# Performance work log

Hardware: AMD Instinct MI355X
Metric: run time of the kernel (lower is better)

Reference implementation:

```python
import jax, jax.numpy as jnp
import numpy as np
from jax.scipy.special import gammaln, logsumexp

S, K, O, H = 64, 16, 32, 30   # state_dim, act_dim, obs_dim, horizon
T, N = 200, 512               # seq len, batch
EPS = 1e-6
LOG2PI = float(np.log(2.0 * np.pi))
NUM_PARAMS = S * O * 2 + K * S * S + S + S + 1


def setup_inputs() -> dict:
    key = jax.random.key(0)
    k1, k2, k3 = jax.random.split(key, 3)
    o = jax.random.normal(k1, (T, N, O), dtype=jnp.float32)
    a = jax.random.randint(k2, (T, N), 0, K)
    theta = jax.random.normal(k3, (N, NUM_PARAMS), dtype=jnp.float32)
    return {"o": o, "a": a, "theta": theta}


def _transform_params(theta):
    sizes = [S * O * 2, K * S * S, S, S, 1]
    idx = np.cumsum(sizes)[:-1]
    tA, tB, tC, tD, ttau = jnp.split(theta, idx, axis=-1)
    A_mean, A_lv = jnp.split(tA, 2, axis=-1)
    A_mean = A_mean.reshape(-1, S, O)
    A_std = jax.nn.softplus(A_lv.reshape(-1, S, O)) + EPS  # rectify
    B = jax.nn.softmax(tB.reshape(-1, K, S, S), axis=-1)
    C = jax.nn.softmax(tC.reshape(-1, 1, S), axis=-1)
    D = jax.nn.softmax(tD.reshape(-1, S), axis=-1)
    tau = jax.nn.sigmoid(ttau) * (2.0 * H) + 1.0  # [N,1]
    return A_mean, A_std, B, C, D, tau


def reference(o, a, theta):
    A_mean, A_std, B, C, D, tau = _transform_params(theta)

    # --- negative expected free energy reward: r[n,k,i] ---
    ent = jnp.sum(0.5 + 0.5 * LOG2PI + jnp.log(A_std), axis=-1)          # Normal entropy, [N,S]
    kl = jnp.sum(B * (jnp.log(B + EPS) - jnp.log(C[:, None] + EPS)), -1)  # KL(B || C), [N,K,S]
    eh = jnp.einsum('nkij,nj->nki', B, ent)
    r = -kl - eh

    # --- finite-horizon value iteration: q [H,N,K,S] ---
    def vi_step(qt, _):
        v = logsumexp(qt, axis=-2)                    # [N,S]
        qn = r + jnp.einsum('nkij,nj->nki', B, v)
        return qn, qn
    _, q_rest = jax.lax.scan(vi_step, r, None, length=H - 1)
    q = jnp.concatenate([r[None], q_rest], axis=0)

    # --- truncated poisson horizon weights: pdf [N,H] ---
    hh = jnp.arange(H, dtype=jnp.float32)
    logp_h = hh[None, :] * jnp.log(tau) - tau - gammaln(hh + 1.0)[None, :]
    pdf = jnp.exp(logp_h)
    pdf = pdf / jnp.sum(pdf, axis=-1, keepdims=True)

    batch_idx = jnp.arange(N)

    def time_step(b, inp):
        o_t, a_t = inp
        # policy from current belief
        qb = jnp.einsum('ni,hnki->hnk', b, q)
        pi_h = jax.nn.softmax(qb, axis=-1)
        pi_t = jnp.einsum('hnk,nh->nk', pi_h, pdf)
        # belief update
        B_a = B[batch_idx, a_t]                       # [N,S,S]
        s = jnp.einsum('nij,ni->nj', B_a, b)
        logp_s = jnp.log(s + EPS)
        lp = -0.5 * ((o_t[:, None, :] - A_mean) / A_std) ** 2 \
             - jnp.log(A_std) - 0.5 * LOG2PI          # [N,S,O]
        joint = logp_s + jnp.sum(lp, axis=-1)         # [N,S]
        b_next = jax.nn.softmax(joint, axis=-1)
        logp_o = logsumexp(joint, axis=-1)
        return b_next, (pi_t, b, logp_o)

    _, (pi, b_seq, logp_o) = jax.lax.scan(time_step, D, (o, a))
    return pi, b_seq, logp_o
```

## Files before the change

### kernel.cpp

```cpp
#include <hip/hip_runtime.h>
#include <hip/hip_bf16.h>
#include <math.h>

#define SDIM 64
#define KDIM 16
#define ODIM 32
#define HDIM 30
#define TDIM 200
#define NDIM 512
#define NP 69761
#define EPSV 1e-6f
#define LOG2PIF 1.8378770664093453f

__device__ __forceinline__ float softplusf(float x) {
    return (x > 0.f) ? x + log1pf(expf(-x)) : log1pf(expf(x));
}
__device__ __forceinline__ float wave_max64(float v) {
#pragma unroll
    for (int off = 32; off; off >>= 1) v = fmaxf(v, __shfl_xor(v, off, 64));
    return v;
}
__device__ __forceinline__ float wave_sum64(float v) {
#pragma unroll
    for (int off = 32; off; off >>= 1) v += __shfl_xor(v, off, 64);
    return v;
}
__device__ __forceinline__ void bar_lds() {
    asm volatile("s_waitcnt lgkmcnt(0)\n\ts_barrier" ::: "memory");
}

__global__ __launch_bounds__(256) void transform_kernel(
    const float* __restrict__ theta, float* __restrict__ invstd,
    float* __restrict__ c0, float* __restrict__ ent,
    float* __restrict__ logC, float* __restrict__ Dws,
    float* __restrict__ pdfws)
{
    __shared__ float ls[SDIM * 33];
    const int n = blockIdx.x, tid = threadIdx.x;
    const float* thn = theta + (size_t)n * NP;

    for (int idx = tid; idx < SDIM * ODIM; idx += 256) {
        float x = thn[2048 + idx];
        float sp = softplusf(x) + EPSV;
        invstd[(size_t)n * SDIM * ODIM + idx] = 1.f / sp;
        int s = idx >> 5, oo = idx & 31;
        ls[s * 33 + oo] = logf(sp);
    }
    __syncthreads();

    const int wave = tid >> 6, lane = tid & 63;
    if (wave == 0) {
        float sum = 0.f;
#pragma unroll
        for (int oo = 0; oo < ODIM; ++oo) sum += ls[lane * 33 + oo];
        c0[n * SDIM + lane]  = -sum - 16.f * LOG2PIF;
        ent[n * SDIM + lane] =  sum + 32.f * (0.5f + 0.5f * LOG2PIF);
    } else if (wave == 1) {
        float x = thn[69632 + lane];
        float m = wave_max64(x);
        float e = expf(x - m);
        float ssum = wave_sum64(e);
        logC[n * SDIM + lane] = logf(e / ssum + EPSV);
    } else if (wave == 2) {
        float x = thn[69696 + lane];
        float m = wave_max64(x);
        float e = expf(x - m);
        float ssum = wave_sum64(e);
        Dws[n * SDIM + lane] = e / ssum;
    } else {
        float tt = thn[69760];
        float tau = 60.f / (1.f + expf(-tt)) + 1.f;
        float p = 0.f;
        if (lane < HDIM)
            p = expf((float)lane * logf(tau) - tau - lgammaf((float)lane + 1.f));
        float ssum = wave_sum64(p);
        if (lane < HDIM) pdfws[n * HDIM + lane] = p / ssum;
    }
}

__global__ __launch_bounds__(256) void row_stats_kernel(
    const float* __restrict__ theta, const float* __restrict__ logC,
    const float* __restrict__ ent, float* __restrict__ lse,
    float* __restrict__ rws, __hip_bfloat16* __restrict__ bn)
{
    const int gw = blockIdx.x * 4 + (threadIdx.x >> 6);
    const int lane = threadIdx.x & 63;
    const int n = gw >> 10, rl = gw & 1023;
    float x = theta[(size_t)n * NP + 4096 + (size_t)rl * 64 + lane];
    float m = wave_max64(x);
    float e = expf(x - m);
    float ssum = wave_sum64(e);
    float Bj = e / ssum;
    if (bn) {
        const int k = rl >> 6, i = rl & 63;
        __hip_bfloat16 h = __float2bfloat16(Bj);
        unsigned short bits;
        __builtin_memcpy(&bits, &h, 2);
        ((unsigned short*)bn)[(size_t)n * KDIM * SDIM * SDIM
            + (size_t)k * 4096 + (size_t)(i >> 1) * 128 + lane * 2 + (i & 1)] = bits;
    }
    float contrib = Bj * (logf(Bj + EPSV) - logC[n * SDIM + lane] + ent[n * SDIM + lane]);
    contrib = wave_sum64(contrib);
    if (lane == 0) {
        lse[gw] = m + logf(ssum);
        rws[gw] = -contrib;
    }
}

#define Z2PART(TT_, BUF_) do {                                                 \
    const int ob_ = (wave - 1) * 8;                                            \
    const float* om_ = &o_s[(TT_) * ODIM + ob_];                               \
    float zz_ = 0.f;                                                           \
    _Pragma("unroll")                                                          \
    for (int j_ = 0; j_ < 8; ++j_) {                                           \
        float z_ = (om_[j_] - mean_s[lane * 33 + ob_ + j_])                    \
                 * istd_s[lane * 33 + ob_ + j_];                               \
        zz_ += z_ * z_;                                                        \
    }                                                                          \
    z2p_s[BUF_][wave - 1][lane] = zz_;                                         \
} while (0)

#define BSTEPF(T_, U_) do {                                                    \
    const int cur_ = (T_) & 1, nxt_ = cur_ ^ 1;                                \
    float ecz_ = 0.f, cm_ = 0.f;                                               \
    if (wave >= 1) {                                                           \
        float aA_ = 0.f, aB_ = 0.f;                                            \
        _Pragma("unroll")                                                      \
        for (int ii = 0; ii < 10; ii += 2) {                                   \
            if (ii < nrow)     aA_ += er[ii]     * b_bc[cur_][rbase + ii];     \
            if (ii + 1 < nrow) aB_ += er[ii + 1] * b_bc[cur_][rbase + ii + 1]; \
        }                                                                      \
        part_s[wave - 1][lane] = aA_ + aB_;                                    \
        if (wave == 6) out_b[((size_t)(T_) * NDIM + n) * SDIM + lane] = b_bc[cur_][lane]; \
    } else {                                                                   \
        float z2_ = z2p_s[cur_][0][lane] + z2p_s[cur_][1][lane]                \
                  + z2p_s[cur_][2][lane] + z2p_s[cur_][3][lane];               \
        float c_ = c0_r - 0.5f * z2_;                                          \
        cm_ = wave_max64(c_);                                                  \
        ecz_ = __expf(c_ - cm_);                                               \
    }                                                                          \
    bar_lds();                                             \
    if (wave == 0) {                                                           \
        float sv_ = part_s[0][lane] + part_s[1][lane] + part_s[2][lane]        \
                  + part_s[3][lane] + part_s[4][lane] + part_s[5][lane]        \
                  + part_s[6][lane];                                           \
        float u_ = (sv_ + EPSV) * ecz_;                                        \
        float S_ = wave_sum64(u_);                                             \
        b_bc[nxt_][lane] = u_ / S_;                                            \
        if (lane == 0) out_lp[(size_t)(T_) * NDIM + n] = cm_ + __logf(S_);     \
    } else {                                                                   \
        if ((T_) + 1 < TDIM) {                                                 \
            _Pragma("unroll")                                                  \
            for (int m_ = 0; m_ < 5; ++m_) {                                   \
                if (2 * m_ < nrow)                                             \
                    er[2 * m_] = __uint_as_float(U_[m_] << 16);                \
                if (2 * m_ + 1 < nrow)                                         \
                    er[2 * m_ + 1] = __uint_as_float(U_[m_] & 0xffff0000u);    \
            }                                                                  \
            if (wave <= 4) Z2PART((T_) + 1, nxt_);                             \
        }                                                                      \
        const int tl_ = ((T_) + 3 < TDIM) ? (T_) + 3 : TDIM - 1;               \
        const uint* up_ = bnn32 + (size_t)a_s[tl_] * 2048 + (rbase >> 1) * 64 + lane; \
        _Pragma("unroll")                                                      \
        for (int m_ = 0; m_ < 5; ++m_)                                         \
            if (2 * m_ < nrow) U_[m_] = up_[m_ * 64];                          \
    }                                                                          \
    bar_lds();                                                 \
} while (0)

__global__ __launch_bounds__(512) void belief_fast_kernel(
    const float* __restrict__ o, const int* __restrict__ a,
    const float* __restrict__ theta, const __hip_bfloat16* __restrict__ bn,
    const float* __restrict__ invstd, const float* __restrict__ c0g,
    const float* __restrict__ Dws,
    float* __restrict__ out_b, float* __restrict__ out_lp)
{
    __shared__ float o_s[TDIM * ODIM];
    __shared__ int   a_s[TDIM];
    __shared__ float mean_s[SDIM * 33];
    __shared__ float istd_s[SDIM * 33];
    __shared__ float c0_sh[SDIM];
    __shared__ __align__(16) float b_bc[2][SDIM];
    __shared__ float part_s[7][68];
    __shared__ float z2p_s[2][4][SDIM];

    const int n = blockIdx.x, tid = threadIdx.x;
    const int wave = tid >> 6, lane = tid & 63;
    const float* thn = theta + (size_t)n * NP;
    const uint* bnn32 = (const uint*)(bn + (size_t)n * KDIM * SDIM * SDIM);

    for (int idx = tid; idx < TDIM * ODIM; idx += 512)
        o_s[idx] = o[((size_t)(idx >> 5) * NDIM + n) * ODIM + (idx & 31)];
    if (tid < TDIM) a_s[tid] = a[tid * NDIM + n];
    for (int idx = tid; idx < SDIM * ODIM; idx += 512) {
        int s = idx >> 5, oo = idx & 31;
        mean_s[s * 33 + oo] = thn[idx];
        istd_s[s * 33 + oo] = invstd[(size_t)n * SDIM * ODIM + idx];
    }
    if (tid < SDIM) { c0_sh[tid] = c0g[n * SDIM + tid]; b_bc[0][tid] = Dws[n * SDIM + tid]; }
    __syncthreads();

    const float c0_r = (wave == 0) ? c0_sh[lane] : 0.f;
    const int rbase = (wave >= 1) ? (wave - 1) * 10 : 0;
    const int nrow  = (wave >= 1) ? ((SDIM - rbase) < 10 ? (SDIM - rbase) : 10) : 0;

    float er[10];
    uint u0[5], u1[5];
    if (wave >= 1) {
        const uint* p0 = bnn32 + (size_t)a_s[0] * 2048 + (rbase >> 1) * 64 + lane;
#pragma unroll
        for (int m = 0; m < 5; ++m) if (2 * m < nrow) u0[m] = p0[m * 64];
#pragma unroll
        for (int m = 0; m < 5; ++m) {
            if (2 * m < nrow)     er[2 * m]     = __uint_as_float(u0[m] << 16);
            if (2 * m + 1 < nrow) er[2 * m + 1] = __uint_as_float(u0[m] & 0xffff0000u);
        }
        const uint* p1 = bnn32 + (size_t)a_s[1] * 2048 + (rbase >> 1) * 64 + lane;
#pragma unroll
        for (int m = 0; m < 5; ++m) if (2 * m < nrow) u0[m] = p1[m * 64];
        const uint* p2 = bnn32 + (size_t)a_s[2] * 2048 + (rbase >> 1) * 64 + lane;
#pragma unroll
        for (int m = 0; m < 5; ++m) if (2 * m < nrow) u1[m] = p2[m * 64];
        if (wave <= 4) Z2PART(0, 0);
    }
    __syncthreads();

#pragma unroll 1
    for (int t = 0; t < TDIM; t += 2) {
        BSTEPF(t, u0);
        BSTEPF(t + 1, u1);
    }
}

#define BSTEP(T_, RAW_) do {                                                   \
    const int cur_ = (T_) & 1, nxt_ = cur_ ^ 1;                                \
    if (wave >= 1) {                                                           \
        float acc_ = 0.f;                                                      \
        _Pragma("unroll")                                                      \
        for (int ii = 0; ii < 10; ++ii)                                        \
            if (ii < nrow) acc_ += er[ii] * b_s[cur_][rbase + ii];             \
        part_s[wave - 1][lane] = acc_;                                         \
        if (wave == 6) out_b[((size_t)(T_) * NDIM + n) * SDIM + lane] = b_s[cur_][lane]; \
    }                                                                          \
    bar_lds();                                                                 \
    if (wave == 0) {                                                           \
        float sv_ = part_s[0][lane] + part_s[1][lane] + part_s[2][lane]        \
                  + part_s[3][lane] + part_s[4][lane] + part_s[5][lane]        \
                  + part_s[6][lane];                                           \
        float z2_ = z2p_s[cur_][0][lane] + z2p_s[cur_][1][lane]                \
                  + z2p_s[cur_][2][lane] + z2p_s[cur_][3][lane];               \
        float joint_ = __logf(sv_ + EPSV) + c0_s[lane] - 0.5f * z2_;           \
        float m_ = wave_max64(joint_);                                         \
        float e_ = __expf(joint_ - m_);                                        \
        float ss_ = wave_sum64(e_);                                            \
        b_s[nxt_][lane] = e_ / ss_;                                            \
        if (lane == 0) out_lp[(size_t)(T_) * NDIM + n] = m_ + __logf(ss_);     \
    } else {                                                                   \
        if ((T_) + 1 < TDIM) {                                                 \
            const int an_ = a_s[(T_) + 1];                                     \
            const float* ln_ = lseA + an_ * SDIM;                              \
            _Pragma("unroll")                                                  \
            for (int ii = 0; ii < 10; ++ii)                                    \
                if (ii < nrow) er[ii] = __expf(RAW_[ii] - ln_[rbase + ii]);    \
            if (wave <= 4) Z2PART((T_) + 1, nxt_);                             \
        }                                                                      \
        const int tl_ = ((T_) + 3 < TDIM) ? (T_) + 3 : TDIM - 1;               \
        const int a3_ = a_s[tl_];                                              \
        const float* X3_ = Xn + (size_t)a3_ * SDIM * SDIM;                     \
        _Pragma("unroll")                                                      \
        for (int ii = 0; ii < 10; ++ii)                                        \
            if (ii < nrow) RAW_[ii] = X3_[(size_t)(rbase + ii) * SDIM + lane]; \
    }                                                                          \
    bar_lds();                                                                 \
} while (0)

__global__ __launch_bounds__(512) void belief_kernel(
    const float* __restrict__ o, const int* __restrict__ a,
    const float* __restrict__ theta, const float* __restrict__ lse,
    const float* __restrict__ invstd, const float* __restrict__ c0g,
    const float* __restrict__ Dws,
    float* __restrict__ out_b, float* __restrict__ out_lp)
{
    __shared__ float o_s[TDIM * ODIM];
    __shared__ int   a_s[TDIM];
    __shared__ float mean_s[SDIM * 33];
    __shared__ float istd_s[SDIM * 33];
    __shared__ float lseA[KDIM * SDIM];
    __shared__ float c0_s[SDIM];
    __shared__ float b_s[2][SDIM];
    __shared__ float part_s[7][68];
    __shared__ float z2p_s[2][4][SDIM];

    const int n = blockIdx.x, tid = threadIdx.x;
    const int wave = tid >> 6, lane = tid & 63;
    const float* thn = theta + (size_t)n * NP;
    const float* Xn  = thn + 4096;

    for (int idx = tid; idx < TDIM * ODIM; idx += 512)
        o_s[idx] = o[((size_t)(idx >> 5) * NDIM + n) * ODIM + (idx & 31)];
    if (tid < TDIM) a_s[tid] = a[tid * NDIM + n];
    for (int idx = tid; idx < SDIM * ODIM; idx += 512) {
        int s = idx >> 5, oo = idx & 31;
        mean_s[s * 33 + oo] = thn[idx];
        istd_s[s * 33 + oo] = invstd[(size_t)n * SDIM * ODIM + idx];
    }
    for (int idx = tid; idx < KDIM * SDIM; idx += 512)
        lseA[idx] = lse[(size_t)n * KDIM * SDIM + idx];
    if (tid < SDIM) { c0_s[tid] = c0g[n * SDIM + tid]; b_s[0][tid] = Dws[n * SDIM + tid]; }
    __syncthreads();

    const int rbase = (wave >= 1) ? (wave - 1) * 10 : 0;
    const int nrow  = (wave >= 1) ? ((SDIM - rbase) < 10 ? (SDIM - rbase) : 10) : 0;

    float er[10], raw0[10], raw1[10];
    if (wave >= 1) {
        const int a0 = a_s[0];
        const float* X0 = Xn + (size_t)a0 * SDIM * SDIM;
        const float* l0 = lseA + a0 * SDIM;
#pragma unroll
        for (int ii = 0; ii < 10; ++ii)
            if (ii < nrow) er[ii] = __expf(X0[(size_t)(rbase + ii) * SDIM + lane] - l0[rbase + ii]);
        const int a1 = a_s[1];
        const float* X1 = Xn + (size_t)a1 * SDIM * SDIM;
#pragma unroll
        for (int ii = 0; ii < 10; ++ii)
            if (ii < nrow) raw0[ii] = X1[(size_t)(rbase + ii) * SDIM + lane];
        const int a2 = a_s[2];
        const float* X2 = Xn + (size_t)a2 * SDIM * SDIM;
#pragma unroll
        for (int ii = 0; ii < 10; ++ii)
            if (ii < nrow) raw1[ii] = X2[(size_t)(rbase + ii) * SDIM + lane];
        if (wave <= 4) Z2PART(0, 0);
    }
    __syncthreads();

#pragma unroll 1
    for (int t = 0; t < TDIM; t += 2) {
        BSTEP(t, raw0);
        BSTEP(t + 1, raw1);
    }
}

__global__ __launch_bounds__(512) void vi_kernel(
    const float* __restrict__ theta, const float* __restrict__ lse,
    const float* __restrict__ rws, float* __restrict__ q_ws)
{
    __shared__ float q_lds[KDIM * 68];
    __shared__ __align__(16) float v_lds[68];
    const int n = blockIdx.x, tid = threadIdx.x;
    const float* Xn = theta + (size_t)n * NP + 4096;

    const float l0  = lse[(size_t)n * 1024 + tid];
    const float l1  = lse[(size_t)n * 1024 + 512 + tid];
    const float rr0 = rws[(size_t)n * 1024 + tid];
    const float rr1 = rws[(size_t)n * 1024 + 512 + tid];

    float4 er0[16], er1[16];
    {
        const float* X0 = Xn + (size_t)tid * 64;
        const float* X1 = Xn + (size_t)(512 + tid) * 64;
#pragma unroll
        for (int j = 0; j < 16; ++j) {
            float4 x = *(const float4*)(X0 + j * 4);
            er0[j] = make_float4(__expf(x.x - l0), __expf(x.y - l0),
                                 __expf(x.z - l0), __expf(x.w - l0));
            float4 y = *(const float4*)(X1 + j * 4);
            er1[j] = make_float4(__expf(y.x - l1), __expf(y.y - l1),
                                 __expf(y.z - l1), __expf(y.w - l1));
        }
    }

    float qr0 = rr0, qr1 = rr1;
    float* qw = q_ws + (size_t)n * HDIM * 1024;
    const int kq0 = tid >> 6, iq = tid & 63;
    qw[tid] = qr0;
    qw[512 + tid] = qr1;
    q_lds[kq0 * 68 + iq] = qr0;
    q_lds[(8 + kq0) * 68 + iq] = qr1;
    __syncthreads();

#pragma unroll 1
    for (int h = 1; h < HDIM; ++h) {
        if (tid < 64) {
            float m = -1e30f;
#pragma unroll
            for (int k = 0; k < KDIM; ++k) m = fmaxf(m, q_lds[k * 68 + tid]);
            float s = 0.f;
#pragma unroll
            for (int k = 0; k < KDIM; ++k) s += __expf(q_lds[k * 68 + tid] - m);
            v_lds[tid] = m + __logf(s);
        }
        bar_lds();
        float a0x = 0.f, a0y = 0.f, a0z = 0.f, a0w = 0.f;
        float a1x = 0.f, a1y = 0.f, a1z = 0.f, a1w = 0.f;
#pragma unroll
        for (int jq = 0; jq < 16; ++jq) {
            const float4 v4 = *(const float4*)&v_lds[jq * 4];
            a0x += er0[jq].x * v4.x; a0y += er0[jq].y * v4.y;
            a0z += er0[jq].z * v4.z; a0w += er0[jq].w * v4.w;
            a1x += er1[jq].x * v4.x; a1y += er1[jq].y * v4.y;
            a1z += er1[jq].z * v4.z; a1w += er1[jq].w * v4.w;
        }
        qr0 = rr0 + ((a0x + a0y) + (a0z + a0w));
        qr1 = rr1 + ((a1x + a1y) + (a1z + a1w));
        qw[(size_t)h * 1024 + tid] = qr0;
        qw[(size_t)h * 1024 + 512 + tid] = qr1;
        q_lds[kq0 * 68 + iq] = qr0;
        q_lds[(8 + kq0) * 68 + iq] = qr1;
        bar_lds();
    }
}

__global__ __launch_bounds__(512, 1) void policy_bc_kernel(
    const float* __restrict__ q_ws, const float* __restrict__ out_b_g,
    const float* __restrict__ pdfg, float* __restrict__ out_pi)
{
    __shared__ __align__(16) float b_all[TDIM * SDIM];
    __shared__ float part[2][8][16];
    __shared__ float pdf_s[32];

    const int n = blockIdx.x, tid = threadIdx.x;
    const int w = tid >> 6, lane = tid & 63;
    const int hl = lane >> 4, kk = lane & 15;
    const int hown = w * 4 + hl;
    const float* qn = q_ws + (size_t)n * HDIM * 1024;

    for (int idx = tid; idx < TDIM * 16; idx += 512) {
        const int t = idx >> 4, jq = idx & 15;
        *(float4*)&b_all[t * SDIM + jq * 4] =
            *(const float4*)&out_b_g[((size_t)t * NDIM + n) * SDIM + jq * 4];
    }
    if (tid < 32) pdf_s[tid] = (tid < HDIM) ? pdfg[n * HDIM + tid] : 0.f;

    float4 qrow[16];
    if (hown < HDIM) {
#pragma unroll
        for (int jq = 0; jq < 16; ++jq)
            qrow[jq] = *(const float4*)&qn[(size_t)hown * 1024 + kk * 64 + jq * 4];
    } else {
#pragma unroll
        for (int jq = 0; jq < 16; ++jq)
            qrow[jq] = make_float4(0.f, 0.f, 0.f, 0.f);
    }
    __syncthreads();
    const float pdfh = pdf_s[hown];

#pragma unroll 1
    for (int t = 0; t < TDIM; ++t) {
        const int cur = t & 1;
        const float* br = &b_all[t * SDIM];
        float ax = 0.f, ay = 0.f, az = 0.f, aw = 0.f;
#pragma unroll
        for (int jq = 0; jq < 16; ++jq) {
            const float4 b4 = *(const float4*)&br[jq * 4];
            ax += qrow[jq].x * b4.x; ay += qrow[jq].y * b4.y;
            az += qrow[jq].z * b4.z; aw += qrow[jq].w * b4.w;
        }
        float acc = (ax + ay) + (az + aw);
        float m = acc;
        m = fmaxf(m, __shfl_xor(m, 1, 64));
        m = fmaxf(m, __shfl_xor(m, 2, 64));
        m = fmaxf(m, __shfl_xor(m, 4, 64));
        m = fmaxf(m, __shfl_xor(m, 8, 64));
        float e = __expf(acc - m);
        float S = e;
        S += __shfl_xor(S, 1, 64);
        S += __shfl_xor(S, 2, 64);
        S += __shfl_xor(S, 4, 64);
        S += __shfl_xor(S, 8, 64);
        float val = pdfh * e / S;
        val += __shfl_xor(val, 16, 64);
        val += __shfl_xor(val, 32, 64);
        if (lane < 16) part[cur][w][lane] = val;
        if (w == 0 && t > 0 && lane < 16) {
            const int prv = cur ^ 1;
            float s8 = 0.f;
#pragma unroll
            for (int ww = 0; ww < 8; ++ww) s8 += part[prv][ww][lane];
            out_pi[((size_t)(t - 1) * NDIM + n) * KDIM + lane] = s8;
        }
        bar_lds();
    }
    if (w == 0 && lane < 16) {
        float s8 = 0.f;
#pragma unroll
        for (int ww = 0; ww < 8; ++ww) s8 += part[(TDIM - 1) & 1][ww][lane];
        out_pi[((size_t)(TDIM - 1) * NDIM + n) * KDIM + lane] = s8;
    }
}

__global__ __launch_bounds__(512) void vi_policy_kernel(
    const float* __restrict__ theta, const float* __restrict__ lse,
    const float* __restrict__ rws, const float* __restrict__ pdfg,
    const float* __restrict__ out_b_g, float* __restrict__ out_pi)
{
    __shared__ __align__(16) float q_s[HDIM * KDIM * 68];
    __shared__ float r_s[KDIM * SDIM];
    __shared__ float lse_s[KDIM * SDIM];
    __shared__ __align__(16) float v_s[SDIM];
    __shared__ __align__(16) float b_lds[64 * 68];
    __shared__ float pdf_s[32];

    const int n = blockIdx.x, tid = threadIdx.x;
    const int wave = tid >> 6, lane = tid & 63;
    const int sub = lane & 15, rq = lane >> 4;
    const float* Xn = theta + (size_t)n * NP + 4096;

    for (int idx = tid; idx < KDIM * SDIM; idx += 512) {
        r_s[idx]   = rws[(size_t)n * KDIM * SDIM + idx];
        lse_s[idx] = lse[(size_t)n * KDIM * SDIM + idx];
    }
    if (tid < HDIM) pdf_s[tid] = pdfg[n * HDIM + tid];
    __syncthreads();

    for (int idx = tid; idx < KDIM * SDIM; idx += 512)
        q_s[(idx >> 6) * 68 + (idx & 63)] = r_s[idx];

    float4 breg[32];
#pragma unroll
    for (int it = 0; it < 32; ++it) {
        const int row = it * 32 + wave * 4 + rq;
        const float* xr = Xn + (size_t)row * SDIM + sub * 4;
        const float l = lse_s[row];
        breg[it] = make_float4(__expf(xr[0] - l), __expf(xr[1] - l),
                               __expf(xr[2] - l), __expf(xr[3] - l));
    }
    bar_lds();

#pragma unroll 1
    for (int h = 1; h < HDIM; ++h) {
        if (tid < SDIM) {
            const int base = (h - 1) * KDIM;
            float m = -1e30f;
#pragma unroll
            for (int k = 0; k < KDIM; ++k) m = fmaxf(m, q_s[(base + k) * 68 + tid]);
            float ssum = 0.f;
#pragma unroll
            for (int k = 0; k < KDIM; ++k) ssum += __expf(q_s[(base + k) * 68 + tid] - m);
            v_s[tid] = m + __logf(ssum);
        }
        bar_lds();
        const float4 v4 = *(const float4*)&v_s[sub * 4];
#pragma unroll
        for (int it = 0; it < 32; ++it) {
            const int row = it * 32 + wave * 4 + rq;
            float acc = breg[it].x * v4.x + breg[it].y * v4.y
                      + breg[it].z * v4.z + breg[it].w * v4.w;
            acc += __shfl_xor(acc, 1, 64);
            acc += __shfl_xor(acc, 2, 64);
            acc += __shfl_xor(acc, 4, 64);
            acc += __shfl_xor(acc, 8, 64);
            if (sub == 0)
                q_s[(h * KDIM + (row >> 6)) * 68 + (row & 63)] = r_s[row] + acc;
        }
        bar_lds();
    }

    const int tc = tid >> 4, kk = tid & 15;
#pragma unroll 1
    for (int t0 = 0; t0 < TDIM; t0 += 64) {
        const int nt = (TDIM - t0) < 64 ? (TDIM - t0) : 64;
        for (int idx = tid; idx < nt * 16; idx += 512) {
            const int row = idx >> 4, jq = idx & 15;
            *(float4*)&b_lds[row * 68 + jq * 4] =
                *(const float4*)&out_b_g[(((size_t)(t0 + row)) * NDIM + n) * SDIM + jq * 4];
        }
        bar_lds();
        const bool vA = tc < nt, vB = (tc + 32) < nt;
        float4 bqA[16], bqB[16];
        if (vA) {
#pragma unroll
            for (int jq = 0; jq < 16; ++jq)
                bqA[jq] = *(const float4*)&b_lds[tc * 68 + jq * 4];
        }
        if (vB) {
#pragma unroll
            for (int jq = 0; jq < 16; ++jq)
                bqB[jq] = *(const float4*)&b_lds[(tc + 32) * 68 + jq * 4];
        }
        float pikA = 0.f, pikB = 0.f;
#pragma unroll 1
        for (int h = 0; h < HDIM; ++h) {
            const float* qr = &q_s[(h * KDIM + kk) * 68];
            float aA = 0.f, aB = 0.f;
#pragma unroll
            for (int jq = 0; jq < 16; ++jq) {
                const float4 qv = *(const float4*)&qr[jq * 4];
                if (vA) aA += qv.x * bqA[jq].x + qv.y * bqA[jq].y
                            + qv.z * bqA[jq].z + qv.w * bqA[jq].w;
                if (vB) aB += qv.x * bqB[jq].x + qv.y * bqB[jq].y
                            + qv.z * bqB[jq].z + qv.w * bqB[jq].w;
            }
            float mA = aA, mB = aB;
            mA = fmaxf(mA, __shfl_xor(mA, 1, 64));
            mA = fmaxf(mA, __shfl_xor(mA, 2, 64));
            mA = fmaxf(mA, __shfl_xor(mA, 4, 64));
            mA = fmaxf(mA, __shfl_xor(mA, 8, 64));
            mB = fmaxf(mB, __shfl_xor(mB, 1, 64));
            mB = fmaxf(mB, __shfl_xor(mB, 2, 64));
            mB = fmaxf(mB, __shfl_xor(mB, 4, 64));
            mB = fmaxf(mB, __shfl_xor(mB, 8, 64));
            float eA = __expf(aA - mA), eB = __expf(aB - mB);
            float SA = eA, SB = eB;
            SA += __shfl_xor(SA, 1, 64);
            SA += __shfl_xor(SA, 2, 64);
            SA += __shfl_xor(SA, 4, 64);
            SA += __shfl_xor(SA, 8, 64);
            SB += __shfl_xor(SB, 1, 64);
            SB += __shfl_xor(SB, 2, 64);
            SB += __shfl_xor(SB, 4, 64);
            SB += __shfl_xor(SB, 8, 64);
            const float ph = pdf_s[h];
            pikA += ph * eA / SA;
            pikB += ph * eB / SB;
        }
        if (vA) out_pi[(((size_t)(t0 + tc)) * NDIM + n) * KDIM + kk] = pikA;
        if (vB) out_pi[(((size_t)(t0 + 32 + tc)) * NDIM + n) * KDIM + kk] = pikB;
        bar_lds();
    }
}

extern "C" void kernel_launch(void* const* d_in, const int* in_sizes, int n_in,
                              void* d_out, int out_size, void* d_ws, size_t ws_size,
                              hipStream_t stream) {
    (void)in_sizes; (void)n_in; (void)out_size;
    const float* o     = (const float*)d_in[0];
    const int*   a     = (const int*)d_in[1];
    const float* theta = (const float*)d_in[2];
    float* out = (float*)d_out;
    float* ws  = (float*)d_ws;

    float* lse    = ws;
    float* rws    = lse    + (size_t)NDIM * KDIM * SDIM;
    float* invstd = rws    + (size_t)NDIM * KDIM * SDIM;
    float* c0     = invstd + (size_t)NDIM * SDIM * ODIM;
    float* ent    = c0     + (size_t)NDIM * SDIM;
    float* logC   = ent    + (size_t)NDIM * SDIM;
    float* Dws    = logC   + (size_t)NDIM * SDIM;
    float* pdfws  = Dws    + (size_t)NDIM * SDIM;
    float* q_ws   = pdfws  + (size_t)NDIM * HDIM;
    __hip_bfloat16* bn = (__hip_bfloat16*)(q_ws + (size_t)NDIM * HDIM * KDIM * SDIM);

    const size_t f_base = (size_t)NDIM * KDIM * SDIM * 2
                        + (size_t)NDIM * SDIM * ODIM
                        + (size_t)NDIM * SDIM * 4
                        + (size_t)NDIM * HDIM;
    const size_t f_q  = (size_t)NDIM * HDIM * KDIM * SDIM;
    const size_t need2 = (f_base + f_q) * 4;
    const size_t need1 = need2 + (size_t)NDIM * KDIM * SDIM * SDIM * 2;

    float* out_pi = out;
    float* out_b  = out + (size_t)TDIM * NDIM * KDIM;
    float* out_lp = out + (size_t)TDIM * NDIM * KDIM + (size_t)TDIM * NDIM * SDIM;

    transform_kernel<<<NDIM, 256, 0, stream>>>(theta, invstd, c0, ent, logC, Dws, pdfws);

    if (ws_size >= need1) {
        row_stats_kernel<<<(NDIM * KDIM * SDIM) / 4, 256, 0, stream>>>(
            theta, logC, ent, lse, rws, bn);
        belief_fast_kernel<<<NDIM, 512, 0, stream>>>(
            o, a, theta, bn, invstd, c0, Dws, out_b, out_lp);
        vi_kernel<<<NDIM, 512, 0, stream>>>(theta, lse, rws, q_ws);
        policy_bc_kernel<<<NDIM, 512, 0, stream>>>(q_ws, out_b, pdfws, out_pi);
    } else if (ws_size >= need2) {
        row_stats_kernel<<<(NDIM * KDIM * SDIM) / 4, 256, 0, stream>>>(
            theta, logC, ent, lse, rws, (__hip_bfloat16*)nullptr);
        belief_kernel<<<NDIM, 512, 0, stream>>>(
            o, a, theta, lse, invstd, c0, Dws, out_b, out_lp);
        vi_kernel<<<NDIM, 512, 0, stream>>>(theta, lse, rws, q_ws);
        policy_bc_kernel<<<NDIM, 512, 0, stream>>>(q_ws, out_b, pdfws, out_pi);
    } else {
        row_stats_kernel<<<(NDIM * KDIM * SDIM) / 4, 256, 0, stream>>>(
            theta, logC, ent, lse, rws, (__hip_bfloat16*)nullptr);
        belief_kernel<<<NDIM, 512, 0, stream>>>(
            o, a, theta, lse, invstd, c0, Dws, out_b, out_lp);
        vi_policy_kernel<<<NDIM, 512, 0, stream>>>(theta, lse, rws, pdfws, out_b, out_pi);
    }
}
```

Baseline: 671.3 us.

## Use symmetric per-wave belief recurrence with one barrier, batch policy steps in pairs

The belief kernel drops the dedicated reduction wave and spreads the 64-row matvec evenly over all 8 waves, 8 rows each. Every wave redundantly does the softmax normalisation and keeps its own copy of the belief, which cuts the per-step barriers from two to one. The policy kernel handles two timesteps per barrier, with a double-buffered partial array. The cost is duplicated exp and reduction work in every wave, plus a larger part_s buffer.

Measured after the change: 659.0 us. Within noise of the previous version (-1.8%).

```diff
diff --git a/kernel.cpp b/kernel.cpp
--- a/kernel.cpp
+++ b/kernel.cpp
@@ -107,68 +107,62 @@
     }
 }
 
-#define Z2PART(TT_, BUF_) do {                                                 \
-    const int ob_ = (wave - 1) * 8;                                            \
-    const float* om_ = &o_s[(TT_) * ODIM + ob_];                               \
-    float zz_ = 0.f;                                                           \
-    _Pragma("unroll")                                                          \
-    for (int j_ = 0; j_ < 8; ++j_) {                                           \
-        float z_ = (om_[j_] - mean_s[lane * 33 + ob_ + j_])                    \
-                 * istd_s[lane * 33 + ob_ + j_];                               \
-        zz_ += z_ * z_;                                                        \
-    }                                                                          \
-    z2p_s[BUF_][wave - 1][lane] = zz_;                                         \
-} while (0)
-
-#define BSTEPF(T_, U_) do {                                                    \
+#define BSYM(T_, U_) do {                                                      \
     const int cur_ = (T_) & 1, nxt_ = cur_ ^ 1;                                \
-    float ecz_ = 0.f, cm_ = 0.f;                                               \
-    if (wave >= 1) {                                                           \
-        float aA_ = 0.f, aB_ = 0.f;                                            \
+    {                \
+        const float4 b0_ = *(const float4*)&b_buf[wave][rbase];                \
+        const float4 b1_ = *(const float4*)&b_buf[wave][rbase + 4];            \
+        float accA_ = er[0] * b0_.x + er[1] * b0_.y + er[2] * b0_.z + er[3] * b0_.w; \
+        float accB_ = er[4] * b1_.x + er[5] * b1_.y + er[6] * b1_.z + er[7] * b1_.w; \
+        part_s[cur_][wave][lane] = accA_ + accB_;                              \
+    }                                                                          \
+    if (wave == 7) out_b[((size_t)(T_) * NDIM + n) * SDIM + lane] = b_buf[7][lane]; \
+    if ((T_) + 1 < TDIM && wave < 4) {                 \
+        const int ob_ = wave * 8;                                              \
+        const float* om_ = &o_s[((T_) + 1) * ODIM + ob_];                      \
+        float zz_ = 0.f;                                                       \
         _Pragma("unroll")                                                      \
-        for (int ii = 0; ii < 10; ii += 2) {                                   \
-            if (ii < nrow)     aA_ += er[ii]     * b_bc[cur_][rbase + ii];     \
-            if (ii + 1 < nrow) aB_ += er[ii + 1] * b_bc[cur_][rbase + ii + 1]; \
+        for (int j_ = 0; j_ < 8; ++j_) {                                       \
+            float z_ = (om_[j_] - mean_s[lane * 33 + ob_ + j_])                \
+                     * istd_s[lane * 33 + ob_ + j_];                           \
+            zz_ += z_ * z_;                                                    \
         }                                                                      \
-        part_s[wave - 1][lane] = aA_ + aB_;                                    \
-        if (wave == 6) out_b[((size_t)(T_) * NDIM + n) * SDIM + lane] = b_bc[cur_][lane]; \
-    } else {                                                                   \
-        float z2_ = z2p_s[cur_][0][lane] + z2p_s[cur_][1][lane]                \
-                  + z2p_s[cur_][2][lane] + z2p_s[cur_][3][lane];               \
-        float c_ = c0_r - 0.5f * z2_;                                          \
-        cm_ = wave_max64(c_);                                                  \
-        ecz_ = __expf(c_ - cm_);                                               \
-    }                                                                          \
-    bar_lds();                                             \
-    if (wave == 0) {                                                           \
-        float sv_ = part_s[0][lane] + part_s[1][lane] + part_s[2][lane]        \
-                  + part_s[3][lane] + part_s[4][lane] + part_s[5][lane]        \
-                  + part_s[6][lane];                                           \
-        float u_ = (sv_ + EPSV) * ecz_;                                        \
-        float S_ = wave_sum64(u_);                                             \
-        b_bc[nxt_][lane] = u_ / S_;                                            \
-        if (lane == 0) out_lp[(size_t)(T_) * NDIM + n] = cm_ + __logf(S_);     \
-    } else {                                                                   \
-        if ((T_) + 1 < TDIM) {                                                 \
-            _Pragma("unroll")                                                  \
-            for (int m_ = 0; m_ < 5; ++m_) {                                   \
-                if (2 * m_ < nrow)                                             \
-                    er[2 * m_] = __uint_as_float(U_[m_] << 16);                \
-                if (2 * m_ + 1 < nrow)                                         \
-                    er[2 * m_ + 1] = __uint_as_float(U_[m_] & 0xffff0000u);    \
-            }                                                                  \
-            if (wave <= 4) Z2PART((T_) + 1, nxt_);                             \
+        z2p_s[nxt_][wave][lane] = zz_;                                         \
+    }                                                                          \
+        \
+    const float z2_ = z2p_s[cur_][0][lane] + z2p_s[cur_][1][lane]              \
+                    + z2p_s[cur_][2][lane] + z2p_s[cur_][3][lane];             \
+    const float c_ = c0_r - 0.5f * z2_;                                        \
+    const float cm_ = wave_max64(c_);                                          \
+    const float ecz_ = __expf(c_ - cm_);                                       \
+    if ((T_) + 1 < TDIM) {                        \
+        _Pragma("unroll")                                                      \
+        for (int m_ = 0; m_ < 4; ++m_) {                                       \
+            er[2 * m_]     = __uint_as_float(U_[m_] << 16);                    \
+            er[2 * m_ + 1] = __uint_as_float(U_[m_] & 0xffff0000u);            \
         }                                                                      \
+    }                                                                          \
+    {                                                 \
         const int tl_ = ((T_) + 3 < TDIM) ? (T_) + 3 : TDIM - 1;               \
         const uint* up_ = bnn32 + (size_t)a_s[tl_] * 2048 + (rbase >> 1) * 64 + lane; \
         _Pragma("unroll")                                                      \
-        for (int m_ = 0; m_ < 5; ++m_)                                         \
-            if (2 * m_ < nrow) U_[m_] = up_[m_ * 64];                          \
-    }                                                                          \
-    bar_lds();                                                 \
+        for (int m_ = 0; m_ < 4; ++m_) U_[m_] = up_[m_ * 64];                  \
+    }                                                                          \
+    bar_lds();                                            \
+    {                                   \
+        float sv_ = part_s[cur_][0][lane] + part_s[cur_][1][lane]              \
+                  + part_s[cur_][2][lane] + part_s[cur_][3][lane]              \
+                  + part_s[cur_][4][lane] + part_s[cur_][5][lane]              \
+                  + part_s[cur_][6][lane] + part_s[cur_][7][lane];             \
+        float u_ = (sv_ + EPSV) * ecz_;                                        \
+        float S_ = wave_sum64(u_);                                             \
+        b_buf[wave][lane] = u_ / S_;                                           \
+        if (wave == 0 && lane == 0)                                            \
+            out_lp[(size_t)(T_) * NDIM + n] = cm_ + __logf(S_);                \
+    }                                                                          \
 } while (0)
 
-__global__ __launch_bounds__(512) void belief_fast_kernel(
+__global__ __launch_bounds__(512) void belief_sym_kernel(
     const float* __restrict__ o, const int* __restrict__ a,
     const float* __restrict__ theta, const __hip_bfloat16* __restrict__ bn,
     const float* __restrict__ invstd, const float* __restrict__ c0g,
@@ -180,12 +174,13 @@
     __shared__ float mean_s[SDIM * 33];
     __shared__ float istd_s[SDIM * 33];
     __shared__ float c0_sh[SDIM];
-    __shared__ __align__(16) float b_bc[2][SDIM];
-    __shared__ float part_s[7][68];
+    __shared__ __align__(16) float b_buf[8][SDIM];
+    __shared__ float part_s[2][8][68];
     __shared__ float z2p_s[2][4][SDIM];
 
     const int n = blockIdx.x, tid = threadIdx.x;
     const int wave = tid >> 6, lane = tid & 63;
+    const int rbase = wave * 8;
     const float* thn = theta + (size_t)n * NP;
     const uint* bnn32 = (const uint*)(bn + (size_t)n * KDIM * SDIM * SDIM);
 
@@ -197,40 +192,62 @@
         mean_s[s * 33 + oo] = thn[idx];
         istd_s[s * 33 + oo] = invstd[(size_t)n * SDIM * ODIM + idx];
     }
-    if (tid < SDIM) { c0_sh[tid] = c0g[n * SDIM + tid]; b_bc[0][tid] = Dws[n * SDIM + tid]; }
+    if (tid < SDIM) c0_sh[tid] = c0g[n * SDIM + tid];
+    b_buf[wave][lane] = Dws[n * SDIM + lane];
     __syncthreads();
 
-    const float c0_r = (wave == 0) ? c0_sh[lane] : 0.f;
-    const int rbase = (wave >= 1) ? (wave - 1) * 10 : 0;
-    const int nrow  = (wave >= 1) ? ((SDIM - rbase) < 10 ? (SDIM - rbase) : 10) : 0;
-
-    float er[10];
-    uint u0[5], u1[5];
-    if (wave >= 1) {
+    const float c0_r = c0_sh[lane];
+
+    float er[8];
+    uint u0[4], u1[4];
+    {
         const uint* p0 = bnn32 + (size_t)a_s[0] * 2048 + (rbase >> 1) * 64 + lane;
 #pragma unroll
-        for (int m = 0; m < 5; ++m) if (2 * m < nrow) u0[m] = p0[m * 64];
-#pragma unroll
-        for (int m = 0; m < 5; ++m) {
-            if (2 * m < nrow)     er[2 * m]     = __uint_as_float(u0[m] << 16);
-            if (2 * m + 1 < nrow) er[2 * m + 1] = __uint_as_float(u0[m] & 0xffff0000u);
+        for (int m = 0; m < 4; ++m) u0[m] = p0[m * 64];
+#pragma unroll
+        for (int m = 0; m < 4; ++m) {
+            er[2 * m]     = __uint_as_float(u0[m] << 16);
+            er[2 * m + 1] = __uint_as_float(u0[m] & 0xffff0000u);
         }
         const uint* p1 = bnn32 + (size_t)a_s[1] * 2048 + (rbase >> 1) * 64 + lane;
 #pragma unroll
-        for (int m = 0; m < 5; ++m) if (2 * m < nrow) u0[m] = p1[m * 64];
+        for (int m = 0; m < 4; ++m) u0[m] = p1[m * 64];
         const uint* p2 = bnn32 + (size_t)a_s[2] * 2048 + (rbase >> 1) * 64 + lane;
 #pragma unroll
-        for (int m = 0; m < 5; ++m) if (2 * m < nrow) u1[m] = p2[m * 64];
-        if (wave <= 4) Z2PART(0, 0);
+        for (int m = 0; m < 4; ++m) u1[m] = p2[m * 64];
+        if (wave < 4) {
+            const int ob = wave * 8;
+            const float* om = &o_s[ob];
+            float zz = 0.f;
+#pragma unroll
+            for (int j = 0; j < 8; ++j) {
+                float z = (om[j] - mean_s[lane * 33 + ob + j]) * istd_s[lane * 33 + ob + j];
+                zz += z * z;
+            }
+            z2p_s[0][wave][lane] = zz;
+        }
     }
     __syncthreads();
 
 #pragma unroll 1
     for (int t = 0; t < TDIM; t += 2) {
-        BSTEPF(t, u0);
-        BSTEPF(t + 1, u1);
-    }
-}
+        BSYM(t, u0);
+        BSYM(t + 1, u1);
+    }
+}
+
+#define Z2PART(TT_, BUF_) do {                                                 \
+    const int ob_ = (wave - 1) * 8;                                            \
+    const float* om_ = &o_s[(TT_) * ODIM + ob_];                               \
+    float zz_ = 0.f;                                                           \
+    _Pragma("unroll")                                                          \
+    for (int j_ = 0; j_ < 8; ++j_) {                                           \
+        float z_ = (om_[j_] - mean_s[lane * 33 + ob_ + j_])                    \
+                 * istd_s[lane * 33 + ob_ + j_];                               \
+        zz_ += z_ * z_;                                                        \
+    }                                                                          \
+    z2p_s[BUF_][wave - 1][lane] = zz_;                                         \
+} while (0)
 
 #define BSTEP(T_, RAW_) do {                                                   \
     const int cur_ = (T_) & 1, nxt_ = cur_ ^ 1;                                \
@@ -416,7 +433,7 @@
     const float* __restrict__ pdfg, float* __restrict__ out_pi)
 {
     __shared__ __align__(16) float b_all[TDIM * SDIM];
-    __shared__ float part[2][8][16];
+    __shared__ float part[2][2][8][16];
     __shared__ float pdf_s[32];
 
     const int n = blockIdx.x, tid = threadIdx.x;
@@ -445,48 +462,52 @@
     __syncthreads();
     const float pdfh = pdf_s[hown];
 
+#define PVAL(T_, OUTV_) do {                                                   \
+    const float* br_ = &b_all[(T_) * SDIM];                                    \
+    float ax_ = 0.f, ay_ = 0.f, az_ = 0.f, aw_ = 0.f;                          \
+    _Pragma("unroll")                                                          \
+    for (int jq_ = 0; jq_ < 16; ++jq_) {                                       \
+        const float4 b4_ = *(const float4*)&br_[jq_ * 4];                      \
+        ax_ += qrow[jq_].x * b4_.x; ay_ += qrow[jq_].y * b4_.y;                \
+        az_ += qrow[jq_].z * b4_.z; aw_ += qrow[jq_].w * b4_.w;                \
+    }                                                                          \
+    float acc_ = (ax_ + ay_) + (az_ + aw_);                                    \
+    float m_ = acc_;                                                           \
+    m_ = fmaxf(m_, __shfl_xor(m_, 1, 64));                                     \
+    m_ = fmaxf(m_, __shfl_xor(m_, 2, 64));                                     \
+    m_ = fmaxf(m_, __shfl_xor(m_, 4, 64));                                     \
+    m_ = fmaxf(m_, __shfl_xor(m_, 8, 64));                                     \
+    float e_ = __expf(acc_ - m_);                                              \
+    float S_ = e_;                                                             \
+    S_ += __shfl_xor(S_, 1, 64);                                               \
+    S_ += __shfl_xor(S_, 2, 64);                                               \
+    S_ += __shfl_xor(S_, 4, 64);                                               \
+    S_ += __shfl_xor(S_, 8, 64);                                               \
+    float v_ = pdfh * e_ / S_;                                                 \
+    v_ += __shfl_xor(v_, 16, 64);                                              \
+    v_ += __shfl_xor(v_, 32, 64);                                              \
+    OUTV_ = v_;                                                                \
+} while (0)
+
 #pragma unroll 1
-    for (int t = 0; t < TDIM; ++t) {
-        const int cur = t & 1;
-        const float* br = &b_all[t * SDIM];
-        float ax = 0.f, ay = 0.f, az = 0.f, aw = 0.f;
-#pragma unroll
-        for (int jq = 0; jq < 16; ++jq) {
-            const float4 b4 = *(const float4*)&br[jq * 4];
-            ax += qrow[jq].x * b4.x; ay += qrow[jq].y * b4.y;
-            az += qrow[jq].z * b4.z; aw += qrow[jq].w * b4.w;
-        }
-        float acc = (ax + ay) + (az + aw);
-        float m = acc;
-        m = fmaxf(m, __shfl_xor(m, 1, 64));
-        m = fmaxf(m, __shfl_xor(m, 2, 64));
-        m = fmaxf(m, __shfl_xor(m, 4, 64));
-        m = fmaxf(m, __shfl_xor(m, 8, 64));
-        float e = __expf(acc - m);
-        float S = e;
-        S += __shfl_xor(S, 1, 64);
-        S += __shfl_xor(S, 2, 64);
-        S += __shfl_xor(S, 4, 64);
-        S += __shfl_xor(S, 8, 64);
-        float val = pdfh * e / S;
-        val += __shfl_xor(val, 16, 64);
-        val += __shfl_xor(val, 32, 64);
-        if (lane < 16) part[cur][w][lane] = val;
-        if (w == 0 && t > 0 && lane < 16) {
-            const int prv = cur ^ 1;
+    for (int t0 = 0; t0 < TDIM; t0 += 2) {
+        const int buf = (t0 >> 1) & 1;
+        float v0, v1;
+        PVAL(t0, v0);
+        PVAL(t0 + 1, v1);
+        if (lane < 16) {
+            part[buf][0][w][lane] = v0;
+            part[buf][1][w][lane] = v1;
+        }
+        bar_lds();
+        if (w < 2 && lane < 16) {
             float s8 = 0.f;
 #pragma unroll
-            for (int ww = 0; ww < 8; ++ww) s8 += part[prv][ww][lane];
-            out_pi[((size_t)(t - 1) * NDIM + n) * KDIM + lane] = s8;
-        }
-        bar_lds();
-    }
-    if (w == 0 && lane < 16) {
-        float s8 = 0.f;
-#pragma unroll
-        for (int ww = 0; ww < 8; ++ww) s8 += part[(TDIM - 1) & 1][ww][lane];
-        out_pi[((size_t)(TDIM - 1) * NDIM + n) * KDIM + lane] = s8;
-    }
+            for (int ww = 0; ww < 8; ++ww) s8 += part[buf][w][ww][lane];
+            out_pi[((size_t)(t0 + w) * NDIM + n) * KDIM + lane] = s8;
+        }
+    }
+#undef PVAL
 }
 
 __global__ __launch_bounds__(512) void vi_policy_kernel(
@@ -658,7 +679,7 @@
     if (ws_size >= need1) {
         row_stats_kernel<<<(NDIM * KDIM * SDIM) / 4, 256, 0, stream>>>(
             theta, logC, ent, lse, rws, bn);
-        belief_fast_kernel<<<NDIM, 512, 0, stream>>>(
+        belief_sym_kernel<<<NDIM, 512, 0, stream>>>(
             o, a, theta, bn, invstd, c0, Dws, out_b, out_lp);
         vi_kernel<<<NDIM, 512, 0, stream>>>(theta, lse, rws, q_ws);
         policy_bc_kernel<<<NDIM, 512, 0, stream>>>(q_ws, out_b, pdfws, out_pi);
```
